# Kernel tuning notes

Hardware: AMD Instinct MI355X
Metric: run time of the kernel (lower is better)

The kernel has to match this reference:

```python
import jax, jax.numpy as jnp
import numpy as np
from jax import lax

HID = 128      # GNN hidden dim (node_label_embedding_size)
EMB = 64       # char-CNN output (graph_node_label_representation_size)
N_LAYERS = 6
N_ETYPES = 12
CHAR_EMB = 16
KW = 5         # conv kernel width
LEAKY = 0.2


def _gru(x, h, k, rk, b):
    # keras-style GRU cell: gates z, r, candidate hh; new h = z*h + (1-z)*hh
    H = h.shape[-1]
    g = x @ k + b                       # [N, 3H]
    z = jax.nn.sigmoid(g[:, :H] + h @ rk[:, :H])
    r = jax.nn.sigmoid(g[:, H:2 * H] + h @ rk[:, H:2 * H])
    hh = jnp.tanh(g[:, 2 * H:] + (r * h) @ rk[:, 2 * H:])
    return z * h + (1.0 - z) * hh


def setup_inputs() -> dict:
    key = jax.random.key(0)
    ks = jax.random.split(key, 32)
    N, U, L, E, G = 100000, 20000, 16, 100000, 64
    inp = {}
    inp["graphs_in_batch"] = G
    inp["node_labels_unique"] = jax.random.randint(ks[0], (U, L), 0, 256, dtype=jnp.int32)
    inp["node_labels_index"] = jax.random.randint(ks[1], (N,), 0, U, dtype=jnp.int32)
    inp["node_to_graph"] = jnp.sort(jax.random.randint(ks[2], (N,), 0, G, dtype=jnp.int32))
    inp["regression_labels"] = jax.random.normal(ks[3], (G,), dtype=jnp.float32)
    for t in range(N_ETYPES):
        inp[f"adj_{t}"] = jax.random.randint(ks[4 + t], (E, 2), 0, N, dtype=jnp.int32)
    # learned params
    inp["char_embed"] = jax.random.normal(ks[16], (256, CHAR_EMB), dtype=jnp.float32) * 0.1
    inp["conv_w"] = jax.random.normal(ks[17], (KW, CHAR_EMB, EMB), dtype=jnp.float32) / np.sqrt(KW * CHAR_EMB)
    inp["conv_b"] = jnp.zeros((EMB,), dtype=jnp.float32)
    inp["W_msg"] = jax.random.normal(ks[18], (N_LAYERS, N_ETYPES, HID, HID), dtype=jnp.float32) / np.sqrt(HID)
    inp["gru_k"] = jax.random.normal(ks[19], (N_LAYERS, HID, 3 * HID), dtype=jnp.float32) / np.sqrt(HID)
    inp["gru_rk"] = jax.random.normal(ks[20], (N_LAYERS, HID, 3 * HID), dtype=jnp.float32) / np.sqrt(HID)
    inp["gru_b"] = jnp.zeros((N_LAYERS, 3 * HID), dtype=jnp.float32)
    inp["score_w"] = jax.random.normal(ks[21], (HID, 1), dtype=jnp.float32) / np.sqrt(HID)
    inp["score_b"] = jnp.zeros((1,), dtype=jnp.float32)
    inp["mlp_w1"] = jax.random.normal(ks[22], (HID, 128), dtype=jnp.float32) / np.sqrt(HID)
    inp["mlp_b1"] = jnp.zeros((128,), dtype=jnp.float32)
    inp["mlp_w2"] = jax.random.normal(ks[23], (128, 32), dtype=jnp.float32) / np.sqrt(128)
    inp["mlp_b2"] = jnp.zeros((32,), dtype=jnp.float32)
    inp["mlp_w3"] = jax.random.normal(ks[24], (32, 8), dtype=jnp.float32) / np.sqrt(32)
    inp["mlp_b3"] = jnp.zeros((8,), dtype=jnp.float32)
    inp["mlp_w4"] = jax.random.normal(ks[25], (8, 1), dtype=jnp.float32) / np.sqrt(8)
    inp["mlp_b4"] = jnp.zeros((1,), dtype=jnp.float32)
    return inp


def reference(graphs_in_batch, node_labels_unique, node_labels_index, node_to_graph,
              regression_labels, adj_0, adj_1, adj_2, adj_3, adj_4, adj_5, adj_6,
              adj_7, adj_8, adj_9, adj_10, adj_11, char_embed, conv_w, conv_b,
              W_msg, gru_k, gru_rk, gru_b, score_w, score_b,
              mlp_w1, mlp_b1, mlp_w2, mlp_b2, mlp_w3, mlp_b3, mlp_w4, mlp_b4):
    adj = jnp.stack([adj_0, adj_1, adj_2, adj_3, adj_4, adj_5, adj_6,
                     adj_7, adj_8, adj_9, adj_10, adj_11])  # [T, E, 2]
    # --- char-CNN node label embedding ---
    chars = char_embed[node_labels_unique]                  # [U, L, CE]
    conv = lax.conv_general_dilated(chars, conv_w, (1,), 'SAME',
                                    dimension_numbers=('NWC', 'WIO', 'NWC'))
    label_rep = jnp.max(jax.nn.relu(conv + conv_b), axis=1)  # [U, EMB]
    feats = label_rep[node_labels_index]                     # [N, EMB]
    N = feats.shape[0]
    # pad initial features up to hidden_dim
    h = jnp.pad(feats, ((0, 0), (0, HID - EMB)))             # [N, HID]
    src = adj[:, :, 0]                                       # [T, E]
    tgt = adj[:, :, 1].reshape(-1)                           # [T*E]
    # --- 6-layer GGNN message passing ---
    for layer in range(N_LAYERS):
        h_src = h[src]                                       # [T, E, HID]
        msgs = jnp.einsum('teh,thd->ted', h_src, W_msg[layer])
        agg = jax.ops.segment_sum(msgs.reshape(-1, HID), tgt, num_segments=N)
        h = _gru(agg, h, gru_k[layer], gru_rk[layer], gru_b[layer])
    # --- weighted-sum graph readout (sigmoid weights, leaky_relu MLP) ---
    scores = jax.nn.sigmoid(h @ score_w + score_b)           # [N, 1]
    v = jax.nn.leaky_relu(h @ mlp_w1 + mlp_b1, LEAKY)
    v = jax.nn.leaky_relu(v @ mlp_w2 + mlp_b2, LEAKY)
    v = jax.nn.leaky_relu(v @ mlp_w3 + mlp_b3, LEAKY)
    v = v @ mlp_w4 + mlp_b4                                  # [N, 1]
    graph_rep = jax.ops.segment_sum(scores * v, node_to_graph,
                                    num_segments=graphs_in_batch)  # [G, 1]
    return graph_rep
```

## Files before the change

### kernel.cpp

```cpp
#include <hip/hip_runtime.h>
#include <hip/hip_bf16.h>

#define LEAKY_SLOPE 0.2f

typedef short short8 __attribute__((ext_vector_type(8)));
typedef float f32x4 __attribute__((ext_vector_type(4)));

static inline int cdiv(int a, int b) { return (a + b - 1) / b; }

__device__ __forceinline__ float bf2f(unsigned short s) {
    return __uint_as_float(((unsigned int)s) << 16);
}
__device__ __forceinline__ unsigned short f2bf(float x) {
    unsigned int u = __float_as_uint(x);
    return (unsigned short)((u + 0x7FFFu + ((u >> 16) & 1u)) >> 16);
}
__device__ __forceinline__ unsigned short bf_hi(float x, float& rem) {
    unsigned int u = __float_as_uint(x);
    unsigned int hi = (u + 0x7FFFu + ((u >> 16) & 1u)) & 0xFFFF0000u;
    rem = x - __uint_as_float(hi);
    return (unsigned short)(hi >> 16);
}

struct EdgeArgs {
    const int* adj[12];
    int E[12];
    int colOff[12];
};
struct ColPtrs { const int* c[12]; };

__global__ __launch_bounds__(64) void label_kernel(
    const int* __restrict__ labels, const float* __restrict__ char_embed,
    const float* __restrict__ conv_w, const float* __restrict__ conv_b,
    float* __restrict__ lr, int U)
{
    __shared__ float ch[20][16];
    __shared__ int lab[16];
    const int u = blockIdx.x, t = threadIdx.x;
    {
        const int r = t >> 4, i = t & 15;
        const int padrow[4] = {0, 1, 18, 19};
        ch[padrow[r]][i] = 0.f;
    }
    if (t < 16) lab[t] = labels[(size_t)u * 16 + t];
    float cwr[5][16];
    #pragma unroll
    for (int k = 0; k < 5; ++k)
        #pragma unroll
        for (int i = 0; i < 16; ++i)
            cwr[k][i] = conv_w[(k * 16 + i) * 64 + t];
    __syncthreads();
    for (int j = t; j < 256; j += 64)
        ch[2 + (j >> 4)][j & 15] = char_embed[(size_t)lab[j >> 4] * 16 + (j & 15)];
    __syncthreads();
    float aw[16];
    const float b = conv_b[t];
    #pragma unroll
    for (int w = 0; w < 16; ++w) aw[w] = b;
    #pragma unroll
    for (int x = 0; x < 20; ++x)
        #pragma unroll
        for (int i = 0; i < 16; ++i) {
            const float chv = ch[x][i];
            #pragma unroll
            for (int k = 0; k < 5; ++k) {
                const int w = x - k;
                if (w >= 0 && w < 16) aw[w] += chv * cwr[k][i];
            }
        }
    float m = 0.f;
    #pragma unroll
    for (int w = 0; w < 16; ++w) m = fmaxf(m, aw[w]);
    lr[(size_t)u * 64 + t] = m;
}

__global__ void init_hP(const int* __restrict__ idx, const float* __restrict__ lr,
                        unsigned short* __restrict__ hP, int N, int NP)
{
    const int i = blockIdx.x * blockDim.x + threadIdx.x;
    if (i >= NP * 16) return;
    const int n = i >> 4, kg = i & 15;
    short8 hi, lo;
    #pragma unroll
    for (int j = 0; j < 8; ++j) { hi[j] = 0; lo[j] = 0; }
    if (n < N && kg < 8) {
        const int id = idx[n];
        #pragma unroll
        for (int j = 0; j < 8; ++j) {
            const float v = lr[(size_t)id * 64 + kg * 8 + j];
            float r; hi[j] = (short)bf_hi(v, r); lo[j] = (short)f2bf(r);
        }
    }
    *(short8*)(hP + (size_t)n * 256 + kg * 16) = hi;
    *(short8*)(hP + (size_t)n * 256 + kg * 16 + 8) = lo;
}

__global__ void hist_kernel(EdgeArgs ea, int* __restrict__ deg, int N)
{
    const int t = blockIdx.y;
    const int e = blockIdx.x * blockDim.x + threadIdx.x;
    if (e >= ea.E[t]) return;
    atomicAdd(&deg[(size_t)t * N + ea.adj[t][2 * e + 1]], 1);
}

__global__ __launch_bounds__(256) void scan_a(const int* __restrict__ deg,
                                              int* __restrict__ partial, int N, int nchunk)
{
    const int t = blockIdx.y, b = blockIdx.x;
    const int base = b * 2048;
    int s = 0;
    for (int i = threadIdx.x; i < 2048; i += 256) {
        const int g = base + i;
        if (g < N) s += deg[(size_t)t * N + g];
    }
    __shared__ int sm[256];
    sm[threadIdx.x] = s; __syncthreads();
    for (int off = 128; off > 0; off >>= 1) {
        if (threadIdx.x < off) sm[threadIdx.x] += sm[threadIdx.x + off];
        __syncthreads();
    }
    if (threadIdx.x == 0) partial[t * nchunk + b] = sm[0];
}

__global__ void scan_b(int* __restrict__ partial, int nchunk)
{
    const int t = threadIdx.x;
    if (t >= 12) return;
    int off = 0;
    for (int i = 0; i < nchunk; ++i) {
        const int s = partial[t * nchunk + i];
        partial[t * nchunk + i] = off;
        off += s;
    }
}

__global__ __launch_bounds__(256) void scan_c(const int* __restrict__ deg,
                                              const int* __restrict__ partial,
                                              int* __restrict__ rowptr, int N, int nchunk)
{
    const int t = blockIdx.y, b = blockIdx.x;
    int* rp = rowptr + (size_t)t * (N + 1);
    const int base = b * 2048;
    int v[8]; int s = 0;
    #pragma unroll
    for (int j = 0; j < 8; ++j) {
        const int g = base + threadIdx.x * 8 + j;
        v[j] = (g < N) ? deg[(size_t)t * N + g] : 0;
        s += v[j];
    }
    __shared__ int ts[256];
    ts[threadIdx.x] = s; __syncthreads();
    for (int off = 1; off < 256; off <<= 1) {
        const int val = (threadIdx.x >= off) ? ts[threadIdx.x - off] : 0;
        __syncthreads();
        ts[threadIdx.x] += val;
        __syncthreads();
    }
    int run = partial[t * nchunk + b] + (threadIdx.x ? ts[threadIdx.x - 1] : 0);
    #pragma unroll
    for (int j = 0; j < 8; ++j) {
        const int g = base + threadIdx.x * 8 + j;
        run += v[j];
        if (g < N) rp[g + 1] = run;
    }
    if (b == 0 && threadIdx.x == 0) rp[0] = 0;
}

__global__ void fill_kernel(EdgeArgs ea, const int* __restrict__ rowptr,
                            int* __restrict__ cursor, int* __restrict__ col, int N)
{
    const int t = blockIdx.y;
    const int e = blockIdx.x * blockDim.x + threadIdx.x;
    if (e >= ea.E[t]) return;
    const int s  = ea.adj[t][2 * e];
    const int tg = ea.adj[t][2 * e + 1];
    const int pos = rowptr[(size_t)t * (N + 1) + tg] + atomicAdd(&cursor[(size_t)t * N + tg], 1);
    col[ea.colOff[t] + pos] = s;
}

struct WSrc { const float* wmsg; const float* gk; const float* grk; const float* w1; };

__global__ void split_w_kernel(WSrc s, unsigned short* __restrict__ wb, int nmat)
{
    const int gidx = blockIdx.x * 256 + threadIdx.x;
    const int m = gidx >> 14, e = gidx & 16383;
    if (m >= nmat) return;
    const int kg = e >> 10, rem = e & 1023, c = rem >> 3, j = rem & 7;
    const int k = kg * 8 + j;
    float x;
    if (m < 72) x = s.wmsg[(size_t)m * 16384 + (size_t)k * 128 + c];
    else if (m < 108) {
        const int g = m - 72, layer = g / 6, r2 = g % 6;
        const float* base = (r2 < 3) ? s.gk : s.grk;
        const int slice = r2 % 3;
        x = base[(size_t)layer * 49152 + (size_t)k * 384 + slice * 128 + c];
    } else x = s.w1[(size_t)k * 128 + c];
    float r; const unsigned short hi = bf_hi(x, r);
    wb[(size_t)m * 32768 + e] = hi;
    wb[(size_t)m * 32768 + 16384 + e] = f2bf(r);
}

__global__ __launch_bounds__(256) void agg_kernel(
    const unsigned short* __restrict__ hP,
    const int* __restrict__ rowptr,
    ColPtrs cps,
    const unsigned short* __restrict__ wbL,
    float* __restrict__ agg, int N)
{
    __shared__ unsigned short lds[2][8192];
    const int tid = threadIdx.x, p = blockIdx.x;
    const int r_loc = tid >> 1;
    const int R = p * 128 + r_loc;
    const int kp = (tid & 1) * 2;
    const int wave = tid >> 6, lane = tid & 63;
    const int wr = wave >> 1, wc = wave & 1, lrow = lane & 15, lkg = lane >> 4;
    f32x4 acc[4][4] = {};
    float ga[2][8];

    auto gather = [&](int s) {
        const int t = s >> 2, q = s & 3;
        #pragma unroll
        for (int pc = 0; pc < 2; ++pc)
            #pragma unroll
            for (int j = 0; j < 8; ++j) ga[pc][j] = 0.f;
        if (R < N) {
            const int rbase = t * (N + 1) + R;
            const int e1 = rowptr[rbase + 1];
            const int* __restrict__ cl = cps.c[t];
            for (int e = rowptr[rbase]; e < e1; ++e) {
                const size_t sb = (size_t)cl[e] * 256 + (size_t)(q * 4 + kp) * 16;
                #pragma unroll
                for (int pc = 0; pc < 2; ++pc) {
                    const short8 hh = *(const short8*)(hP + sb + pc * 16);
                    const short8 hl = *(const short8*)(hP + sb + pc * 16 + 8);
                    #pragma unroll
                    for (int j = 0; j < 8; ++j)
                        ga[pc][j] += bf2f((unsigned short)hh[j]) + bf2f((unsigned short)hl[j]);
                }
            }
        }
    };
    auto stq = [&](int buf) {
        unsigned short* L = lds[buf];
        #pragma unroll
        for (int pc = 0; pc < 2; ++pc) {
            short8 hi, lo;
            #pragma unroll
            for (int j = 0; j < 8; ++j) {
                float rem; hi[j] = (short)bf_hi(ga[pc][j], rem); lo[j] = (short)f2bf(rem);
            }
            const int kgl = kp + pc;
            const int u = (kgl * 1024 + r_loc * 8) ^ (kgl << 3);
            *(short8*)(L + u) = hi;
            *(short8*)(L + u + 4096) = lo;
        }
    };
    auto mfma_q = [&](int buf, int s) {
        const unsigned short* L = lds[buf];
        const unsigned short* __restrict__ B = wbL + (size_t)(s >> 2) * 32768;
        const int q = s & 3;
        short8 ah[4], al[4];
        #pragma unroll
        for (int m = 0; m < 4; ++m) {
            const int u = ((lkg << 10) + (wr * 64 + m * 16 + lrow) * 8) ^ (lkg << 3);
            ah[m] = *(const short8*)(L + u);
            al[m] = *(const short8*)(L + u + 4096);
        }
        #pragma unroll
        for (int n = 0; n < 4; ++n) {
            const int ub = (q * 4 + lkg) * 1024 + (wc * 64 + n * 16 + lrow) * 8;
            const short8 bh = *(const short8*)(B + ub);
            const short8 bl = *(const short8*)(B + ub + 16384);
            #pragma unroll
            for (int m = 0; m < 4; ++m) {
                acc[m][n] = __builtin_amdgcn_mfma_f32_16x16x32_bf16(ah[m], bh, acc[m][n], 0, 0, 0);
                acc[m][n] = __builtin_amdgcn_mfma_f32_16x16x32_bf16(ah[m], bl, acc[m][n], 0, 0, 0);
                acc[m][n] = __builtin_amdgcn_mfma_f32_16x16x32_bf16(al[m], bh, acc[m][n], 0, 0, 0);
            }
        }
    };

    gather(0); stq(0); gather(1);
    __syncthreads();
    #pragma unroll 1
    for (int s = 0; s < 48; ++s) {
        mfma_q(s & 1, s);
        if (s < 47) {
            stq((s + 1) & 1);
            if (s < 46) gather(s + 2);
            __syncthreads();
        }
    }

    #pragma unroll
    for (int m = 0; m < 4; ++m)
        #pragma unroll
        for (int n = 0; n < 4; ++n) {
            const int col = wc * 64 + n * 16 + lrow;
            #pragma unroll
            for (int i = 0; i < 4; ++i) {
                const size_t Rg = (size_t)p * 128 + wr * 64 + m * 16 + lkg * 4 + i;
                agg[Rg * 128 + col] = acc[m][n][i];
            }
        }
}

__global__ __launch_bounds__(256) void zr2_kernel(
    const float* __restrict__ aggf, const unsigned short* __restrict__ hP,
    const unsigned short* __restrict__ k0, const unsigned short* __restrict__ k1,
    const unsigned short* __restrict__ rk0, const unsigned short* __restrict__ rk1,
    const float* __restrict__ bias,
    float* __restrict__ Zf, unsigned short* __restrict__ rhP)
{
    __shared__ unsigned short lds[2][8192];
    const int tid = threadIdx.x, p = blockIdx.x;
    const int wave = tid >> 6, lane = tid & 63;
    const int wr = wave >> 1, wc = wave & 1, lrow = lane & 15, lkg = lane >> 4;
    f32x4 acc[2][4][4] = {};
    float fv[16];
    short8 ph[2], pl[2];

    auto ldq = [&](int s) {
        const int q = s & 3;
        #pragma unroll
        for (int j = 0; j < 2; ++j) {
            const int cid = j * 256 + tid, kgl = cid >> 7, row = cid & 127;
            if (s < 4) {
                const float* a = aggf + ((size_t)p * 128 + row) * 128 + q * 32 + kgl * 8;
                const float4 v0 = *(const float4*)(a);
                const float4 v1 = *(const float4*)(a + 4);
                fv[j*8+0]=v0.x; fv[j*8+1]=v0.y; fv[j*8+2]=v0.z; fv[j*8+3]=v0.w;
                fv[j*8+4]=v1.x; fv[j*8+5]=v1.y; fv[j*8+6]=v1.z; fv[j*8+7]=v1.w;
            } else {
                const unsigned short* hp = hP + ((size_t)p * 128 + row) * 256 + (q * 4 + kgl) * 16;
                ph[j] = *(const short8*)(hp);
                pl[j] = *(const short8*)(hp + 8);
            }
        }
    };
    auto stq = [&](int buf, int s) {
        unsigned short* L = lds[buf];
        #pragma unroll
        for (int j = 0; j < 2; ++j) {
            const int cid = j * 256 + tid, kgl = cid >> 7, row = cid & 127;
            const int u = (kgl * 1024 + row * 8) ^ (kgl << 3);
            short8 hi, lo;
            if (s < 4) {
                #pragma unroll
                for (int q8 = 0; q8 < 8; ++q8) {
                    float rem; hi[q8] = (short)bf_hi(fv[j*8+q8], rem); lo[q8] = (short)f2bf(rem);
                }
            } else { hi = ph[j]; lo = pl[j]; }
            *(short8*)(L + u) = hi;
            *(short8*)(L + u + 4096) = lo;
        }
    };
    auto mfma_q = [&](int buf, int s) {
        const unsigned short* L = lds[buf];
        const int q = s & 3;
        short8 ah[4], al[4];
        #pragma unroll
        for (int m = 0; m < 4; ++m) {
            const int u = ((lkg << 10) + (wr * 64 + m * 16 + lrow) * 8) ^ (lkg << 3);
            ah[m] = *(const short8*)(L + u);
            al[m] = *(const short8*)(L + u + 4096);
        }
        const unsigned short* Bt[2] = { (s < 4) ? k0 : rk0, (s < 4) ? k1 : rk1 };
        #pragma unroll
        for (int t = 0; t < 2; ++t) {
            const unsigned short* __restrict__ B = Bt[t];
            #pragma unroll
            for (int n = 0; n < 4; ++n) {
                const int ub = (q * 4 + lkg) * 1024 + (wc * 64 + n * 16 + lrow) * 8;
                const short8 bh = *(const short8*)(B + ub);
                const short8 bl = *(const short8*)(B + ub + 16384);
                #pragma unroll
                for (int m = 0; m < 4; ++m) {
                    acc[t][m][n] = __builtin_amdgcn_mfma_f32_16x16x32_bf16(ah[m], bh, acc[t][m][n], 0, 0, 0);
                    acc[t][m][n] = __builtin_amdgcn_mfma_f32_16x16x32_bf16(ah[m], bl, acc[t][m][n], 0, 0, 0);
                    acc[t][m][n] = __builtin_amdgcn_mfma_f32_16x16x32_bf16(al[m], bh, acc[t][m][n], 0, 0, 0);
                }
            }
        }
    };

    ldq(0); stq(0, 0); ldq(1);
    __syncthreads();
    #pragma unroll
    for (int s = 0; s < 8; ++s) {
        mfma_q(s & 1, s);
        if (s < 7) {
            stq((s + 1) & 1, s + 1);
            if (s < 6) ldq(s + 2);
            __syncthreads();
        }
    }

    #pragma unroll
    for (int m = 0; m < 4; ++m)
        #pragma unroll
        for (int n = 0; n < 4; ++n) {
            const int col = wc * 64 + n * 16 + lrow;
            #pragma unroll
            for (int i = 0; i < 4; ++i) {
                const int rl = wr * 64 + m * 16 + lkg * 4 + i;
                const size_t R = (size_t)p * 128 + rl;
                const float z = 1.f / (1.f + __expf(-(acc[0][m][n][i] + bias[col])));
                Zf[R * 128 + col] = z;
                const float r = 1.f / (1.f + __expf(-(acc[1][m][n][i] + bias[128 + col])));
                const size_t hu = R * 256 + (size_t)(col >> 3) * 16 + (col & 7);
                const float h = bf2f(hP[hu]) + bf2f(hP[hu + 8]);
                float rem; const unsigned short hh = bf_hi(r * h, rem);
                rhP[hu] = hh;
                rhP[hu + 8] = f2bf(rem);
            }
        }
}

__global__ __launch_bounds__(256) void g2_kernel(
    const float* __restrict__ aggf, const unsigned short* __restrict__ rhP,
    const unsigned short* __restrict__ k2, const unsigned short* __restrict__ rk2,
    const float* __restrict__ bias, const float* __restrict__ Zf,
    unsigned short* __restrict__ hP)
{
    __shared__ unsigned short lds[2][8192];
    const int tid = threadIdx.x, p = blockIdx.x;
    const int wave = tid >> 6, lane = tid & 63;
    const int wr = wave >> 1, wc = wave & 1, lrow = lane & 15, lkg = lane >> 4;
    f32x4 acc[4][4] = {};
    float fv[16];
    short8 ph[2], pl[2];

    auto ldq = [&](int s) {
        const int q = s & 3;
        #pragma unroll
        for (int j = 0; j < 2; ++j) {
            const int cid = j * 256 + tid, kgl = cid >> 7, row = cid & 127;
            if (s < 4) {
                const float* a = aggf + ((size_t)p * 128 + row) * 128 + q * 32 + kgl * 8;
                const float4 v0 = *(const float4*)(a);
                const float4 v1 = *(const float4*)(a + 4);
                fv[j*8+0]=v0.x; fv[j*8+1]=v0.y; fv[j*8+2]=v0.z; fv[j*8+3]=v0.w;
                fv[j*8+4]=v1.x; fv[j*8+5]=v1.y; fv[j*8+6]=v1.z; fv[j*8+7]=v1.w;
            } else {
                const unsigned short* hp = rhP + ((size_t)p * 128 + row) * 256 + (q * 4 + kgl) * 16;
                ph[j] = *(const short8*)(hp);
                pl[j] = *(const short8*)(hp + 8);
            }
        }
    };
    auto stq = [&](int buf, int s) {
        unsigned short* L = lds[buf];
        #pragma unroll
        for (int j = 0; j < 2; ++j) {
            const int cid = j * 256 + tid, kgl = cid >> 7, row = cid & 127;
            const int u = (kgl * 1024 + row * 8) ^ (kgl << 3);
            short8 hi, lo;
            if (s < 4) {
                #pragma unroll
                for (int q8 = 0; q8 < 8; ++q8) {
                    float rem; hi[q8] = (short)bf_hi(fv[j*8+q8], rem); lo[q8] = (short)f2bf(rem);
                }
            } else { hi = ph[j]; lo = pl[j]; }
            *(short8*)(L + u) = hi;
            *(short8*)(L + u + 4096) = lo;
        }
    };
    auto mfma_q = [&](int buf, int s) {
        const unsigned short* L = lds[buf];
        const int q = s & 3;
        short8 ah[4], al[4];
        #pragma unroll
        for (int m = 0; m < 4; ++m) {
            const int u = ((lkg << 10) + (wr * 64 + m * 16 + lrow) * 8) ^ (lkg << 3);
            ah[m] = *(const short8*)(L + u);
            al[m] = *(const short8*)(L + u + 4096);
        }
        const unsigned short* __restrict__ B = (s < 4) ? k2 : rk2;
        #pragma unroll
        for (int n = 0; n < 4; ++n) {
            const int ub = (q * 4 + lkg) * 1024 + (wc * 64 + n * 16 + lrow) * 8;
            const short8 bh = *(const short8*)(B + ub);
            const short8 bl = *(const short8*)(B + ub + 16384);
            #pragma unroll
            for (int m = 0; m < 4; ++m) {
                acc[m][n] = __builtin_amdgcn_mfma_f32_16x16x32_bf16(ah[m], bh, acc[m][n], 0, 0, 0);
                acc[m][n] = __builtin_amdgcn_mfma_f32_16x16x32_bf16(ah[m], bl, acc[m][n], 0, 0, 0);
                acc[m][n] = __builtin_amdgcn_mfma_f32_16x16x32_bf16(al[m], bh, acc[m][n], 0, 0, 0);
            }
        }
    };

    ldq(0); stq(0, 0); ldq(1);
    __syncthreads();
    #pragma unroll
    for (int s = 0; s < 8; ++s) {
        mfma_q(s & 1, s);
        if (s < 7) {
            stq((s + 1) & 1, s + 1);
            if (s < 6) ldq(s + 2);
            __syncthreads();
        }
    }

    #pragma unroll
    for (int m = 0; m < 4; ++m)
        #pragma unroll
        for (int n = 0; n < 4; ++n) {
            const int col = wc * 64 + n * 16 + lrow;
            #pragma unroll
            for (int i = 0; i < 4; ++i) {
                const int rl = wr * 64 + m * 16 + lkg * 4 + i;
                const size_t R = (size_t)p * 128 + rl;
                const float g = acc[m][n][i] + bias[col];
                const size_t hu = R * 256 + (size_t)(col >> 3) * 16 + (col & 7);
                const float h = bf2f(hP[hu]) + bf2f(hP[hu + 8]);
                const float z = Zf[R * 128 + col];
                const float hn = z * h + (1.f - z) * tanhf(g);
                float rem; const unsigned short hh = bf_hi(hn, rem);
                hP[hu] = hh;
                hP[hu + 8] = f2bf(rem);
            }
        }
}

__global__ __launch_bounds__(256) void v1_kernel(
    const unsigned short* __restrict__ hP, const unsigned short* __restrict__ w1b,
    const float* __restrict__ bias, float* __restrict__ outF)
{
    __shared__ unsigned short lds[2][8192];
    const int tid = threadIdx.x, p = blockIdx.x;
    const int wave = tid >> 6, lane = tid & 63;
    const int wr = wave >> 1, wc = wave & 1, lrow = lane & 15, lkg = lane >> 4;
    f32x4 acc[4][4] = {};
    short8 ph[2], pl[2];

    auto ldq = [&](int s) {
        #pragma unroll
        for (int j = 0; j < 2; ++j) {
            const int cid = j * 256 + tid, kgl = cid >> 7, row = cid & 127;
            const unsigned short* hp = hP + ((size_t)p * 128 + row) * 256 + (s * 4 + kgl) * 16;
            ph[j] = *(const short8*)(hp);
            pl[j] = *(const short8*)(hp + 8);
        }
    };
    auto stq = [&](int buf) {
        unsigned short* L = lds[buf];
        #pragma unroll
        for (int j = 0; j < 2; ++j) {
            const int cid = j * 256 + tid, kgl = cid >> 7, row = cid & 127;
            const int u = (kgl * 1024 + row * 8) ^ (kgl << 3);
            *(short8*)(L + u) = ph[j];
            *(short8*)(L + u + 4096) = pl[j];
        }
    };
    auto mfma_q = [&](int buf, int s) {
        const unsigned short* L = lds[buf];
        short8 ah[4], al[4];
        #pragma unroll
        for (int m = 0; m < 4; ++m) {
            const int u = ((lkg << 10) + (wr * 64 + m * 16 + lrow) * 8) ^ (lkg << 3);
            ah[m] = *(const short8*)(L + u);
            al[m] = *(const short8*)(L + u + 4096);
        }
        #pragma unroll
        for (int n = 0; n < 4; ++n) {
            const int ub = (s * 4 + lkg) * 1024 + (wc * 64 + n * 16 + lrow) * 8;
            const short8 bh = *(const short8*)(w1b + ub);
            const short8 bl = *(const short8*)(w1b + ub + 16384);
            #pragma unroll
            for (int m = 0; m < 4; ++m) {
                acc[m][n] = __builtin_amdgcn_mfma_f32_16x16x32_bf16(ah[m], bh, acc[m][n], 0, 0, 0);
                acc[m][n] = __builtin_amdgcn_mfma_f32_16x16x32_bf16(ah[m], bl, acc[m][n], 0, 0, 0);
                acc[m][n] = __builtin_amdgcn_mfma_f32_16x16x32_bf16(al[m], bh, acc[m][n], 0, 0, 0);
            }
        }
    };

    ldq(0); stq(0); ldq(1);
    __syncthreads();
    #pragma unroll
    for (int s = 0; s < 4; ++s) {
        mfma_q(s & 1, s);
        if (s < 3) {
            stq((s + 1) & 1);
            if (s < 2) ldq(s + 2);
            __syncthreads();
        }
    }

    #pragma unroll
    for (int m = 0; m < 4; ++m)
        #pragma unroll
        for (int n = 0; n < 4; ++n) {
            const int col = wc * 64 + n * 16 + lrow;
            #pragma unroll
            for (int i = 0; i < 4; ++i) {
                const size_t R = (size_t)p * 128 + wr * 64 + m * 16 + lkg * 4 + i;
                float v = acc[m][n][i] + bias[col];
                v = v > 0.f ? v : LEAKY_SLOPE * v;
                outF[R * 128 + col] = v;
            }
        }
}

__global__ __launch_bounds__(256) void final_kernel(
    const unsigned short* __restrict__ hP, const float* __restrict__ V1,
    const int* __restrict__ n2g,
    const float* __restrict__ w2, const float* __restrict__ b2,
    const float* __restrict__ w3, const float* __restrict__ b3,
    const float* __restrict__ w4, const float* __restrict__ b4,
    const float* __restrict__ score_w, const float* __restrict__ score_b,
    float* __restrict__ out, int N)
{
    const int n = blockIdx.x * blockDim.x + threadIdx.x;
    const int nc = n < N ? n : N - 1;
    const int g = n2g[nc];

    float sp = score_b[0];
    #pragma unroll 4
    for (int kg = 0; kg < 16; ++kg) {
        const size_t hu = (size_t)nc * 256 + kg * 16;
        const short8 hh = *(const short8*)(hP + hu);
        const short8 hl = *(const short8*)(hP + hu + 8);
        #pragma unroll
        for (int j = 0; j < 8; ++j)
            sp += (bf2f((unsigned short)hh[j]) + bf2f((unsigned short)hl[j])) * score_w[kg * 8 + j];
    }

    float V2[32];
    #pragma unroll
    for (int j = 0; j < 32; ++j) V2[j] = b2[j];
    #pragma unroll 2
    for (int k = 0; k < 128; k += 4) {
        const float4 v1 = *reinterpret_cast<const float4*>(V1 + (size_t)nc * 128 + k);
        const float vv[4] = {v1.x, v1.y, v1.z, v1.w};
        #pragma unroll
        for (int kk = 0; kk < 4; ++kk)
            #pragma unroll
            for (int j = 0; j < 32; ++j)
                V2[j] += vv[kk] * w2[(k + kk) * 32 + j];
    }
    #pragma unroll
    for (int j = 0; j < 32; ++j) { const float x = V2[j]; V2[j] = x > 0.f ? x : LEAKY_SLOPE * x; }

    float V3[8];
    #pragma unroll
    for (int j = 0; j < 8; ++j) V3[j] = b3[j];
    #pragma unroll
    for (int k = 0; k < 32; ++k)
        #pragma unroll
        for (int j = 0; j < 8; ++j) V3[j] += V2[k] * w3[k * 8 + j];
    #pragma unroll
    for (int j = 0; j < 8; ++j) { const float x = V3[j]; V3[j] = x > 0.f ? x : LEAKY_SLOPE * x; }

    float o4 = b4[0];
    #pragma unroll
    for (int j = 0; j < 8; ++j) o4 += V3[j] * w4[j];

    const float sc = 1.f / (1.f + __expf(-sp));
    float val = (n < N) ? sc * o4 : 0.f;

    const int g0 = __shfl(g, 0, 64);
    if (__all(g == g0)) {
        #pragma unroll
        for (int d = 32; d > 0; d >>= 1) val += __shfl_xor(val, d, 64);
        if ((threadIdx.x & 63) == 0) unsafeAtomicAdd(out + g0, val);
    } else {
        if (n < N) unsafeAtomicAdd(out + g, val);
    }
}

extern "C" void kernel_launch(void* const* d_in, const int* in_sizes, int n_in,
                              void* d_out, int out_size, void* d_ws, size_t ws_size,
                              hipStream_t stream)
{
    (void)n_in;
    const int* labels   = (const int*)d_in[1];
    const int* nidx     = (const int*)d_in[2];
    const int* n2g      = (const int*)d_in[3];
    EdgeArgs ea;
    int Emax = 0, Etot = 0;
    for (int t = 0; t < 12; ++t) {
        ea.adj[t] = (const int*)d_in[5 + t];
        ea.E[t] = in_sizes[5 + t] / 2;
        ea.colOff[t] = Etot;
        Etot += ea.E[t];
        if (ea.E[t] > Emax) Emax = ea.E[t];
    }
    const float* char_embed = (const float*)d_in[17];
    const float* conv_w     = (const float*)d_in[18];
    const float* conv_b     = (const float*)d_in[19];
    const float* W_msg      = (const float*)d_in[20];
    const float* gru_k      = (const float*)d_in[21];
    const float* gru_rk     = (const float*)d_in[22];
    const float* gru_b      = (const float*)d_in[23];
    const float* score_w    = (const float*)d_in[24];
    const float* score_b    = (const float*)d_in[25];
    const float* w1 = (const float*)d_in[26];
    const float* b1 = (const float*)d_in[27];
    const float* w2 = (const float*)d_in[28];
    const float* b2 = (const float*)d_in[29];
    const float* w3 = (const float*)d_in[30];
    const float* b3 = (const float*)d_in[31];
    const float* w4 = (const float*)d_in[32];
    const float* b4 = (const float*)d_in[33];

    const int N = in_sizes[2];
    const int U = in_sizes[1] / 16;
    const int G = out_size;
    float* out = (float*)d_out;

    const int NPB = cdiv(N, 128);
    const int NP  = NPB * 128;
    const int NCHUNK = cdiv(N, 2048);
    const int NMAT = 109;

    float* ws = (float*)d_ws;
    size_t o = 0;
    float* lr   = ws + o; o += (size_t)U * 64;
    float* hPf  = ws + o; o += (size_t)NP * 128;
    float* aggf = ws + o; o += (size_t)NP * 128;
    float* Zf   = ws + o; o += (size_t)NP * 128;
    float* rhPf = ws + o; o += (size_t)NP * 128;
    float* wbf  = ws + o; o += (size_t)NMAT * 16384;
    int* rowptr = (int*)(ws + o);
    int* colarr = rowptr + (size_t)12 * (N + 1);
    const size_t total_bytes = o * sizeof(float)
        + ((size_t)12 * (N + 1) + (size_t)Etot) * sizeof(int);
    if (total_bytes > ws_size) return;

    unsigned short* hP  = (unsigned short*)hPf;
    unsigned short* rhP = (unsigned short*)rhPf;
    unsigned short* wb  = (unsigned short*)wbf;

    int* deg     = (int*)Zf;
    int* cursor  = deg + (size_t)12 * N;
    int* partial = cursor + (size_t)12 * N;

    hipMemsetAsync(d_out, 0, (size_t)G * sizeof(float), stream);
    hipMemsetAsync(deg, 0, ((size_t)24 * N + 12 * NCHUNK) * sizeof(int), stream);

    {
        const dim3 ge(cdiv(Emax, 256), 12);
        const dim3 gs(NCHUNK, 12);
        hist_kernel<<<ge, 256, 0, stream>>>(ea, deg, N);
        scan_a<<<gs, 256, 0, stream>>>(deg, partial, N, NCHUNK);
        scan_b<<<1, 64, 0, stream>>>(partial, NCHUNK);
        scan_c<<<gs, 256, 0, stream>>>(deg, partial, rowptr, N, NCHUNK);
        fill_kernel<<<ge, 256, 0, stream>>>(ea, rowptr, cursor, colarr, N);
    }

    WSrc wsrc{W_msg, gru_k, gru_rk, w1};
    split_w_kernel<<<cdiv(NMAT * 16384, 256), 256, 0, stream>>>(wsrc, wb, NMAT);
    label_kernel<<<U, 64, 0, stream>>>(labels, char_embed, conv_w, conv_b, lr, U);
    init_hP<<<cdiv(NP * 16, 256), 256, 0, stream>>>(nidx, lr, hP, N, NP);

    ColPtrs cps;
    for (int t = 0; t < 12; ++t) cps.c[t] = colarr + ea.colOff[t];
    auto wbm = [&](int m) { return wb + (size_t)m * 32768; };

    for (int layer = 0; layer < 6; ++layer) {
        const float* bl = gru_b + (size_t)layer * 384;
        const int mk = 72 + layer * 6;
        agg_kernel<<<NPB, 256, 0, stream>>>(hP, rowptr, cps,
                                            wbm(layer * 12), aggf, N);
        zr2_kernel<<<NPB, 256, 0, stream>>>(aggf, hP, wbm(mk + 0), wbm(mk + 1),
                                            wbm(mk + 3), wbm(mk + 4), bl, Zf, rhP);
        g2_kernel<<<NPB, 256, 0, stream>>>(aggf, rhP, wbm(mk + 2), wbm(mk + 5),
                                           bl + 256, Zf, hP);
    }
    v1_kernel<<<NPB, 256, 0, stream>>>(hP, wbm(108), b1, Zf);
    final_kernel<<<cdiv(N, 256), 256, 0, stream>>>(hP, Zf, n2g, w2, b2, w3, b3, w4, b4,
                                                   score_w, score_b, out, N);
}
```

Before: 4.518 ms.

## Parallelize agg gather over edges with LDS atomic accumulation per edge type

The aggregation kernel no longer has each thread pair walk the edge list of one target row. All edges of a 128-row block are now split across threads (four threads per edge, each covering 32 columns), and the summed features are accumulated into a swizzled fp32 LDS tile with shared-memory atomics. The fill kernel stores a per-edge local row byte so the target row is known without a search. This is meant to remove load imbalance and serial per-row latency from varying in-degrees. In exchange it adds many LDS atomics, a 64KB LDS footprint that lowers occupancy, and loses the previous double-buffered overlap of gather with MFMA.

```diff
diff --git a/kernel.cpp b/kernel.cpp
--- a/kernel.cpp
+++ b/kernel.cpp
@@ -28,6 +28,7 @@
     int colOff[12];
 };
 struct ColPtrs { const int* c[12]; };
+struct TlocPtrs { const unsigned char* c[12]; };
 
 __global__ __launch_bounds__(64) void label_kernel(
     const int* __restrict__ labels, const float* __restrict__ char_embed,
@@ -167,7 +168,8 @@
 }
 
 __global__ void fill_kernel(EdgeArgs ea, const int* __restrict__ rowptr,
-                            int* __restrict__ cursor, int* __restrict__ col, int N)
+                            int* __restrict__ cursor, int* __restrict__ col,
+                            unsigned char* __restrict__ tloc, int N)
 {
     const int t = blockIdx.y;
     const int e = blockIdx.x * blockDim.x + threadIdx.x;
@@ -176,6 +178,7 @@
     const int tg = ea.adj[t][2 * e + 1];
     const int pos = rowptr[(size_t)t * (N + 1) + tg] + atomicAdd(&cursor[(size_t)t * N + tg], 1);
     col[ea.colOff[t] + pos] = s;
+    tloc[ea.colOff[t] + pos] = (unsigned char)(tg & 127);
 }
 
 struct WSrc { const float* wmsg; const float* gk; const float* grk; const float* w1; };
@@ -202,94 +205,92 @@
 
 __global__ __launch_bounds__(256) void agg_kernel(
     const unsigned short* __restrict__ hP,
-    const int* __restrict__ rowptr,
-    ColPtrs cps,
+    const int* __restrict__ rowptr, ColPtrs cps, TlocPtrs tps,
     const unsigned short* __restrict__ wbL,
     float* __restrict__ agg, int N)
 {
-    __shared__ unsigned short lds[2][8192];
+    __shared__ float Sf[16384];
     const int tid = threadIdx.x, p = blockIdx.x;
-    const int r_loc = tid >> 1;
-    const int R = p * 128 + r_loc;
-    const int kp = (tid & 1) * 2;
+    const int R0 = p * 128;
     const int wave = tid >> 6, lane = tid & 63;
     const int wr = wave >> 1, wc = wave & 1, lrow = lane & 15, lkg = lane >> 4;
+    const int j4 = tid & 3;
     f32x4 acc[4][4] = {};
-    float ga[2][8];
-
-    auto gather = [&](int s) {
-        const int t = s >> 2, q = s & 3;
-        #pragma unroll
-        for (int pc = 0; pc < 2; ++pc)
-            #pragma unroll
-            for (int j = 0; j < 8; ++j) ga[pc][j] = 0.f;
-        if (R < N) {
-            const int rbase = t * (N + 1) + R;
-            const int e1 = rowptr[rbase + 1];
+
+    const int rLo = R0 < N ? R0 : N;
+    const int rHi = (R0 + 128) < N ? (R0 + 128) : N;
+
+    for (int t = 0; t < 12; ++t) {
+        {
+            const f32x4 zz = {0.f, 0.f, 0.f, 0.f};
+            #pragma unroll
+            for (int i = 0; i < 16; ++i)
+                *(f32x4*)(Sf + (size_t)(i * 256 + tid) * 4) = zz;
+        }
+        __syncthreads();
+        {
+            const int* __restrict__ rp_t = rowptr + (size_t)t * (N + 1);
+            const int e0 = rp_t[rLo], e1 = rp_t[rHi];
             const int* __restrict__ cl = cps.c[t];
-            for (int e = rowptr[rbase]; e < e1; ++e) {
-                const size_t sb = (size_t)cl[e] * 256 + (size_t)(q * 4 + kp) * 16;
+            const unsigned char* __restrict__ tl = tps.c[t];
+            for (int e = e0 + (tid >> 2); e < e1; e += 64) {
+                const int src = cl[e];
+                const int tr = (int)tl[e];
+                const unsigned short* hp = hP + (size_t)src * 256 + j4 * 64;
                 #pragma unroll
-                for (int pc = 0; pc < 2; ++pc) {
-                    const short8 hh = *(const short8*)(hP + sb + pc * 16);
-                    const short8 hl = *(const short8*)(hP + sb + pc * 16 + 8);
+                for (int kg = 0; kg < 4; ++kg) {
+                    const short8 hh = *(const short8*)(hp + kg * 16);
+                    const short8 hl = *(const short8*)(hp + kg * 16 + 8);
                     #pragma unroll
-                    for (int j = 0; j < 8; ++j)
-                        ga[pc][j] += bf2f((unsigned short)hh[j]) + bf2f((unsigned short)hl[j]);
+                    for (int q = 0; q < 8; ++q) {
+                        const int c = j4 * 32 + kg * 8 + q;
+                        const int fi = tr * 128 + ((((c >> 2) ^ (tr & 7)) << 2) | (c & 3));
+                        atomicAdd(&Sf[fi],
+                                  bf2f((unsigned short)hh[q]) + bf2f((unsigned short)hl[q]));
+                    }
                 }
             }
         }
-    };
-    auto stq = [&](int buf) {
-        unsigned short* L = lds[buf];
-        #pragma unroll
-        for (int pc = 0; pc < 2; ++pc) {
-            short8 hi, lo;
-            #pragma unroll
-            for (int j = 0; j < 8; ++j) {
-                float rem; hi[j] = (short)bf_hi(ga[pc][j], rem); lo[j] = (short)f2bf(rem);
-            }
-            const int kgl = kp + pc;
-            const int u = (kgl * 1024 + r_loc * 8) ^ (kgl << 3);
-            *(short8*)(L + u) = hi;
-            *(short8*)(L + u + 4096) = lo;
-        }
-    };
-    auto mfma_q = [&](int buf, int s) {
-        const unsigned short* L = lds[buf];
-        const unsigned short* __restrict__ B = wbL + (size_t)(s >> 2) * 32768;
-        const int q = s & 3;
-        short8 ah[4], al[4];
-        #pragma unroll
-        for (int m = 0; m < 4; ++m) {
-            const int u = ((lkg << 10) + (wr * 64 + m * 16 + lrow) * 8) ^ (lkg << 3);
-            ah[m] = *(const short8*)(L + u);
-            al[m] = *(const short8*)(L + u + 4096);
-        }
-        #pragma unroll
-        for (int n = 0; n < 4; ++n) {
-            const int ub = (q * 4 + lkg) * 1024 + (wc * 64 + n * 16 + lrow) * 8;
-            const short8 bh = *(const short8*)(B + ub);
-            const short8 bl = *(const short8*)(B + ub + 16384);
-            #pragma unroll
-            for (int m = 0; m < 4; ++m) {
-                acc[m][n] = __builtin_amdgcn_mfma_f32_16x16x32_bf16(ah[m], bh, acc[m][n], 0, 0, 0);
-                acc[m][n] = __builtin_amdgcn_mfma_f32_16x16x32_bf16(ah[m], bl, acc[m][n], 0, 0, 0);
-                acc[m][n] = __builtin_amdgcn_mfma_f32_16x16x32_bf16(al[m], bh, acc[m][n], 0, 0, 0);
-            }
-        }
-    };
-
-    gather(0); stq(0); gather(1);
-    __syncthreads();
-    #pragma unroll 1
-    for (int s = 0; s < 48; ++s) {
-        mfma_q(s & 1, s);
-        if (s < 47) {
-            stq((s + 1) & 1);
-            if (s < 46) gather(s + 2);
-            __syncthreads();
-        }
+        __syncthreads();
+        {
+            const unsigned short* __restrict__ B = wbL + (size_t)t * 32768;
+            #pragma unroll
+            for (int q = 0; q < 4; ++q) {
+                short8 ah[4], al[4];
+                #pragma unroll
+                for (int m = 0; m < 4; ++m) {
+                    const int row = wr * 64 + m * 16 + lrow;
+                    const int g0 = q * 8 + lkg * 2;
+                    const f32x4 x0 = *(const f32x4*)(Sf + row * 128 + ((g0 ^ (row & 7)) << 2));
+                    const f32x4 x1 = *(const f32x4*)(Sf + row * 128 + (((g0 + 1) ^ (row & 7)) << 2));
+                    #pragma unroll
+                    for (int j = 0; j < 4; ++j) {
+                        float rem;
+                        ah[m][j] = (short)bf_hi(x0[j], rem);
+                        al[m][j] = (short)f2bf(rem);
+                    }
+                    #pragma unroll
+                    for (int j = 0; j < 4; ++j) {
+                        float rem;
+                        ah[m][4 + j] = (short)bf_hi(x1[j], rem);
+                        al[m][4 + j] = (short)f2bf(rem);
+                    }
+                }
+                #pragma unroll
+                for (int n = 0; n < 4; ++n) {
+                    const int ub = (q * 4 + lkg) * 1024 + (wc * 64 + n * 16 + lrow) * 8;
+                    const short8 bh = *(const short8*)(B + ub);
+                    const short8 bl = *(const short8*)(B + ub + 16384);
+                    #pragma unroll
+                    for (int m = 0; m < 4; ++m) {
+                        acc[m][n] = __builtin_amdgcn_mfma_f32_16x16x32_bf16(ah[m], bh, acc[m][n], 0, 0, 0);
+                        acc[m][n] = __builtin_amdgcn_mfma_f32_16x16x32_bf16(ah[m], bl, acc[m][n], 0, 0, 0);
+                        acc[m][n] = __builtin_amdgcn_mfma_f32_16x16x32_bf16(al[m], bh, acc[m][n], 0, 0, 0);
+                    }
+                }
+            }
+        }
+        __syncthreads();
     }
 
     #pragma unroll
@@ -726,8 +727,9 @@
     float* wbf  = ws + o; o += (size_t)NMAT * 16384;
     int* rowptr = (int*)(ws + o);
     int* colarr = rowptr + (size_t)12 * (N + 1);
+    unsigned char* tlocarr = (unsigned char*)(colarr + (size_t)Etot);
     const size_t total_bytes = o * sizeof(float)
-        + ((size_t)12 * (N + 1) + (size_t)Etot) * sizeof(int);
+        + ((size_t)12 * (N + 1) + (size_t)Etot) * sizeof(int) + (size_t)Etot;
     if (total_bytes > ws_size) return;
 
     unsigned short* hP  = (unsigned short*)hPf;
@@ -748,7 +750,7 @@
         scan_a<<<gs, 256, 0, stream>>>(deg, partial, N, NCHUNK);
         scan_b<<<1, 64, 0, stream>>>(partial, NCHUNK);
         scan_c<<<gs, 256, 0, stream>>>(deg, partial, rowptr, N, NCHUNK);
-        fill_kernel<<<ge, 256, 0, stream>>>(ea, rowptr, cursor, colarr, N);
+        fill_kernel<<<ge, 256, 0, stream>>>(ea, rowptr, cursor, colarr, tlocarr, N);
     }
 
     WSrc wsrc{W_msg, gru_k, gru_rk, w1};
@@ -757,13 +759,17 @@
     init_hP<<<cdiv(NP * 16, 256), 256, 0, stream>>>(nidx, lr, hP, N, NP);
 
     ColPtrs cps;
-    for (int t = 0; t < 12; ++t) cps.c[t] = colarr + ea.colOff[t];
+    TlocPtrs tps;
+    for (int t = 0; t < 12; ++t) {
+        cps.c[t] = colarr + ea.colOff[t];
+        tps.c[t] = tlocarr + ea.colOff[t];
+    }
     auto wbm = [&](int m) { return wb + (size_t)m * 32768; };
 
     for (int layer = 0; layer < 6; ++layer) {
         const float* bl = gru_b + (size_t)layer * 384;
         const int mk = 72 + layer * 6;
-        agg_kernel<<<NPB, 256, 0, stream>>>(hP, rowptr, cps,
+        agg_kernel<<<NPB, 256, 0, stream>>>(hP, rowptr, cps, tps,
                                             wbm(layer * 12), aggf, N);
         zr2_kernel<<<NPB, 256, 0, stream>>>(aggf, hP, wbm(mk + 0), wbm(mk + 1),
                                             wbm(mk + 3), wbm(mk + 4), bl, Zf, rhP);
```

Result: slower. 8.566 ms (+89.6%).
